# Kernel tuning notes

Measured on AMD Instinct MI355X. Metric: run time of the kernel, lower is better.

Reference implementation:

```python
import jax, jax.numpy as jnp
import numpy as np

B, N, NS, C, H = 2, 2048, 2048, 512, 8
HD = C // H
SCALE = HD ** -0.5
NEG = -10000.0


def setup_inputs() -> dict:
    key = jax.random.key(0)
    ks = jax.random.split(key, 9)
    q = jax.random.normal(ks[0], (B, N, C), dtype=jnp.float32)
    k = jax.random.normal(ks[1], (B, NS, C), dtype=jnp.float32)
    v = jax.random.normal(ks[2], (B, NS, C), dtype=jnp.float32)
    # 1.0 marks invalid support positions (gets -10000 added)
    supp_valid_mask = (jax.random.uniform(ks[3], (B, NS)) < 0.2).astype(jnp.float32)
    # binary fg/bg support mask used for cycle consistency
    supp_mask = jax.random.randint(ks[4], (B, NS), 0, 2, dtype=jnp.int32)
    w = 0.02
    Wq = jax.random.normal(ks[5], (C, C), dtype=jnp.float32) * w
    Wk = jax.random.normal(ks[6], (C, C), dtype=jnp.float32) * w
    Wv = jax.random.normal(ks[7], (C, C), dtype=jnp.float32) * w
    Wproj = jax.random.normal(ks[8], (C, C), dtype=jnp.float32) * w
    return {"q": q, "k": k, "v": v, "supp_valid_mask": supp_valid_mask,
            "supp_mask": supp_mask, "Wq": Wq, "Wk": Wk, "Wv": Wv, "Wproj": Wproj}


def reference(q, k, v, supp_valid_mask, supp_mask, Wq, Wk, Wv, Wproj):
    b, n, c = q.shape
    ns = k.shape[1]
    # linear projections (torch Linear: x @ W^T), split heads -> [B,H,N,HD]
    qh = (q @ Wq.T).reshape(b, n, H, HD).transpose(0, 2, 1, 3)
    kh = (k @ Wk.T).reshape(b, ns, H, HD).transpose(0, 2, 1, 3)
    vh = (v @ Wv.T).reshape(b, ns, H, HD).transpose(0, 2, 1, 3)
    attn = jnp.einsum('bhnd,bhmd->bhnm', qh, kh) * SCALE  # [B,H,N,NS]

    # cycle-consistency association (vectorized over heads)
    k2q = jnp.argmax(attn, axis=2)                    # [B,H,NS] idx into N
    q2k = jnp.argmax(attn, axis=3)                    # [B,H,N]  idx into NS
    re_map_idx = jnp.take_along_axis(q2k, k2q, axis=2)  # [B,H,NS]
    sm = jnp.broadcast_to(supp_mask[:, None, :], (b, H, ns))
    re_map_mask = jnp.take_along_axis(sm, re_map_idx, axis=2)
    asso = sm == re_map_mask                          # [B,H,NS] bool

    # mark cycle-inconsistent positions invalid (eval: ass_drop is identity)
    valid = jnp.broadcast_to(supp_valid_mask[:, None, :], (b, H, ns))
    valid = jnp.where(asso, valid, 1.0)

    attn = attn + (valid * NEG)[:, :, None, :]
    attn = jax.nn.softmax(attn, axis=-1)
    x = jnp.einsum('bhnm,bhmd->bhnd', attn, vh)       # [B,H,N,HD]
    x = x.transpose(0, 2, 1, 3).reshape(b, n, c)
    return x @ Wproj.T
```

## Files before the change

kernel.cpp:

```cpp
#include <hip/hip_runtime.h>
#include <hip/hip_bf16.h>
#include <stdint.h>

#define H_ 8
#define NS_ 2048
#define C_ 512
#define HD_ 64
#define SCALE_ 0.125f
#define NEG_ -10000.0f
#define LOG2E_ 1.4426950408889634f
#define MFIX_ 4.0f

typedef _Float16 f16x8_t __attribute__((ext_vector_type(8)));
typedef _Float16 f16x4_t __attribute__((ext_vector_type(4)));
typedef float f32x4_t __attribute__((ext_vector_type(4)));

#define MFMAH(a, b, c) __builtin_amdgcn_mfma_f32_16x16x32_f16(a, b, c, 0, 0, 0)

__device__ inline f16x8_t load_h8(const _Float16* p) {
    return *reinterpret_cast<const f16x8_t*>(p);
}

__device__ inline void gload_lds16(const void* g, void* l) {
    __builtin_amdgcn_global_load_lds(
        (const __attribute__((address_space(1))) unsigned int*)g,
        (__attribute__((address_space(3))) unsigned int*)l, 16, 0, 0);
}

__device__ inline unsigned orderF(float v) {
    unsigned u = __float_as_uint(v);
    return (u & 0x80000000u) ? ~u : (u | 0x80000000u);
}
__device__ inline unsigned long long packVR(float v, int idx) {
    return ((unsigned long long)orderF(v) << 32) | (unsigned)(~idx);
}
__device__ inline unsigned long long max64(unsigned long long a, unsigned long long b) {
    return a > b ? a : b;
}
__device__ inline unsigned long long shflx64(unsigned long long x, int m) {
    unsigned lo = (unsigned)x, hi = (unsigned)(x >> 32);
    lo = __shfl_xor(lo, m, 64);
    hi = __shfl_xor(hi, m, 64);
    return ((unsigned long long)hi << 32) | lo;
}

__global__ __launch_bounds__(256) void wsplit4(
        const float* __restrict__ w0, const float* __restrict__ w1,
        const float* __restrict__ w2, const float* __restrict__ w3,
        _Float16* __restrict__ hi, _Float16* __restrict__ lo)
{
    const int i = blockIdx.x * 256 + threadIdx.x;
    const int y = blockIdx.y;
    const float* src = (y == 0) ? w0 : (y == 1) ? w1 : (y == 2) ? w2 : w3;
    const float4 v = reinterpret_cast<const float4*>(src)[i];
    f16x4_t hv, lv;
    hv[0] = (_Float16)v.x; hv[1] = (_Float16)v.y;
    hv[2] = (_Float16)v.z; hv[3] = (_Float16)v.w;
    lv[0] = (_Float16)(v.x - (float)hv[0]);
    lv[1] = (_Float16)(v.y - (float)hv[1]);
    lv[2] = (_Float16)(v.z - (float)hv[2]);
    lv[3] = (_Float16)(v.w - (float)hv[3]);
    const size_t o = ((size_t)y << 16) + i;
    reinterpret_cast<f16x4_t*>(hi)[o] = hv;
    reinterpret_cast<f16x4_t*>(lo)[o] = lv;
}

__global__ __launch_bounds__(256) void proj_gemm(
        const float* __restrict__ qin, const float* __restrict__ kin,
        const float* __restrict__ vin,
        const _Float16* __restrict__ wHall, const _Float16* __restrict__ wLall,
        _Float16* __restrict__ qhi, _Float16* __restrict__ qlo,
        _Float16* __restrict__ khi, _Float16* __restrict__ klo,
        _Float16* __restrict__ vT)
{
    __shared__ __attribute__((aligned(16))) _Float16 Wsh[2][2][4096];
    const int zz = blockIdx.z;
    const float* A32 = (zz == 0) ? qin : (zz == 1) ? kin : vin;
    const _Float16* Wh = wHall + ((size_t)zz << 18);
    const _Float16* Wl = wLall + ((size_t)zz << 18);
    const int t = threadIdx.x, w = t >> 6, lane = t & 63;
    const int m16 = lane & 15, quad = lane >> 4;
    const int bm = blockIdx.x << 7, bn = blockIdx.y << 6;
    const int r0 = bm + (w << 5) + m16, r1 = r0 + 16;
    const int krow = lane >> 3, kblk = (lane & 7) ^ (krow & 7);
    const int e = m16 & 7;
    const int s00 = (quad ^ e) << 3, s01 = ((4 + quad) ^ e) << 3;
    const f32x4_t z = {0.f, 0.f, 0.f, 0.f};
    f32x4_t acc[2][4];
    #pragma unroll
    for (int rs = 0; rs < 2; rs++)
        #pragma unroll
        for (int tl = 0; tl < 4; tl++) acc[rs][tl] = z;

    auto stageW = [&](int buf, int kc) {
        #pragma unroll
        for (int ci = 0; ci < 4; ci++) {
            const int pp = (w << 2) + ci;
            const int s = pp >> 3, pj = pp & 7;
            const _Float16* src = (s ? Wl : Wh)
                + (size_t)(bn + (pj << 3) + krow) * C_ + kc + (kblk << 3);
            gload_lds16(src, &Wsh[buf][s][pj << 9]);
        }
    };
    auto loadA = [&](int kc, f16x8_t* d) {
        #pragma unroll
        for (int rs = 0; rs < 2; rs++) {
            const float* pr = A32 + (size_t)(rs ? r1 : r0) * C_ + kc + (quad << 3);
            #pragma unroll
            for (int seg = 0; seg < 2; seg++) {
                f16x8_t hv, lv;
                #pragma unroll
                for (int i = 0; i < 8; i++) {
                    const float x = pr[seg * 32 + i];
                    const _Float16 hh = (_Float16)x;
                    hv[i] = hh;
                    lv[i] = (_Float16)(x - (float)hh);
                }
                d[rs * 4 + seg] = hv;
                d[rs * 4 + seg + 2] = lv;
            }
        }
    };

    f16x8_t cA[8], nA[8];
    stageW(0, 0);
    loadA(0, cA);
    for (int ch = 0; ch < 8; ch++) {
        __syncthreads();
        if (ch + 1 < 8) {
            stageW((ch + 1) & 1, (ch + 1) << 6);
            loadA((ch + 1) << 6, nA);
        }
        const _Float16* W0 = Wsh[ch & 1][0];
        const _Float16* W1 = Wsh[ch & 1][1];
        #pragma unroll
        for (int tl = 0; tl < 4; tl++) {
            const int j64 = ((tl << 4) + m16) << 6;
            const f16x8_t bh0 = load_h8(&W0[j64 + s00]);
            const f16x8_t bh1 = load_h8(&W0[j64 + s01]);
            const f16x8_t bl0 = load_h8(&W1[j64 + s00]);
            const f16x8_t bl1 = load_h8(&W1[j64 + s01]);
            f32x4_t c0 = acc[0][tl];
            c0 = MFMAH(cA[0], bh0, c0); c0 = MFMAH(cA[1], bh1, c0);
            c0 = MFMAH(cA[2], bh0, c0); c0 = MFMAH(cA[3], bh1, c0);
            c0 = MFMAH(cA[0], bl0, c0); c0 = MFMAH(cA[1], bl1, c0);
            acc[0][tl] = c0;
            f32x4_t c1 = acc[1][tl];
            c1 = MFMAH(cA[4], bh0, c1); c1 = MFMAH(cA[5], bh1, c1);
            c1 = MFMAH(cA[6], bh0, c1); c1 = MFMAH(cA[7], bh1, c1);
            c1 = MFMAH(cA[4], bl0, c1); c1 = MFMAH(cA[5], bl1, c1);
            acc[1][tl] = c1;
        }
        #pragma unroll
        for (int i = 0; i < 8; i++) cA[i] = nA[i];
    }
    const int by = blockIdx.y;
    _Float16* o1 = (zz == 0) ? qhi : khi;
    _Float16* o2 = (zz == 0) ? qlo : klo;
    #pragma unroll
    for (int rs = 0; rs < 2; rs++) {
        #pragma unroll
        for (int tl = 0; tl < 4; tl++) {
            #pragma unroll
            for (int r = 0; r < 4; r++) {
                const int gr = bm + (w << 5) + (rs << 4) + (quad << 2) + r;
                const float val = acc[rs][tl][r];
                const int b = gr >> 11, n = gr & 2047;
                const int d = (tl << 4) + m16;
                const int bh = (b << 3) + by;
                if (zz == 2) {
                    vT[(((size_t)((bh << 6) + (n >> 5)) << 6) + d) * 32 + (n & 31)] = (_Float16)val;
                } else {
                    const size_t idx = ((((size_t)bh << 11) + n) << 6) + d;
                    const _Float16 hh = (_Float16)val;
                    o1[idx] = hh;
                    o2[idx] = (_Float16)(val - (float)hh);
                }
            }
        }
    }
}

__global__ __launch_bounds__(256) void argmax_mfma(
        const _Float16* __restrict__ qhi, const _Float16* __restrict__ qlo,
        const _Float16* __restrict__ khi, const _Float16* __restrict__ klo,
        unsigned long long* __restrict__ rowP, unsigned long long* __restrict__ colP)
{
    __shared__ __attribute__((aligned(16))) _Float16 Ksh[2][2][4096];
    __shared__ unsigned long long colbest[1024];
    const int bx = blockIdx.x;
    const int bh = ((bx & 7) << 1) | (bx >> 8);
    const int rt = (bx >> 3) & 15;
    const int ks = (bx >> 7) & 1;
    const int t = threadIdx.x, w = t >> 6, lane = t & 63;
    const int m16 = lane & 15, quad = lane >> 4;
    const int wrow = (rt << 7) + (w << 5);
    const size_t qoff0 = ((((size_t)bh << 11) + wrow + m16) << 6) + (quad << 3);
    const size_t qoff1 = qoff0 + 1024;
    const f16x8_t a00h = load_h8(qhi + qoff0), a01h = load_h8(qhi + qoff0 + 32);
    const f16x8_t a00l = load_h8(qlo + qoff0), a01l = load_h8(qlo + qoff0 + 32);
    const f16x8_t a10h = load_h8(qhi + qoff1), a11h = load_h8(qhi + qoff1 + 32);
    const f16x8_t a10l = load_h8(qlo + qoff1), a11l = load_h8(qlo + qoff1 + 32);
    for (int c = t; c < 1024; c += 256) colbest[c] = 0;
    const int krow = lane >> 3, kblk = (lane & 7) ^ (krow & 7);
    const int e = m16 & 7;
    const int s00 = (quad ^ e) << 3, s01 = ((4 + quad) ^ e) << 3;
    const size_t kbase = (((size_t)bh << 11) + (ks << 10)) << 6;
    float bv0[4] = {-3.4e38f, -3.4e38f, -3.4e38f, -3.4e38f};
    float bv1[4] = {-3.4e38f, -3.4e38f, -3.4e38f, -3.4e38f};
    int bc0[4] = {0, 0, 0, 0}, bc1[4] = {0, 0, 0, 0};
    const f32x4_t z = {0.f, 0.f, 0.f, 0.f};

    auto stage = [&](int buf, int cidx) {
        const size_t ce = kbase + ((size_t)cidx << 12);
        #pragma unroll
        for (int ci = 0; ci < 4; ci++) {
            const int pp = (w << 2) + ci;
            const int s = pp >> 3, pj = pp & 7;
            const _Float16* src = (s ? klo : khi) + ce + (((pj << 3) + krow) << 6) + (kblk << 3);
            gload_lds16(src, &Ksh[buf][s][pj << 9]);
        }
    };

    stage(0, 0);
    for (int ch = 0; ch < 16; ch++) {
        __syncthreads();
        if (ch + 1 < 16) stage((ch + 1) & 1, ch + 1);
        const _Float16* K0 = Ksh[ch & 1][0];
        const _Float16* K1 = Ksh[ch & 1][1];
        const int kc0 = (ks << 10) + (ch << 6);
        #pragma unroll
        for (int tl = 0; tl < 4; tl++) {
            const int j64 = ((tl << 4) + m16) << 6;
            const f16x8_t bh0 = load_h8(&K0[j64 + s00]);
            const f16x8_t bh1 = load_h8(&K0[j64 + s01]);
            const f16x8_t bl0 = load_h8(&K1[j64 + s00]);
            const f16x8_t bl1 = load_h8(&K1[j64 + s01]);
            f32x4_t c0 = MFMAH(a00h, bh0, z);
            c0 = MFMAH(a01h, bh1, c0);
            c0 = MFMAH(a00l, bh0, c0); c0 = MFMAH(a01l, bh1, c0);
            c0 = MFMAH(a00h, bl0, c0); c0 = MFMAH(a01h, bl1, c0);
            f32x4_t c1 = MFMAH(a10h, bh0, z);
            c1 = MFMAH(a11h, bh1, c1);
            c1 = MFMAH(a10l, bh0, c1); c1 = MFMAH(a11l, bh1, c1);
            c1 = MFMAH(a10h, bl0, c1); c1 = MFMAH(a11h, bl1, c1);
            const int gc = kc0 + (tl << 4) + m16;
            #pragma unroll
            for (int r = 0; r < 4; r++) {
                if (c0[r] > bv0[r]) { bv0[r] = c0[r]; bc0[r] = gc; }
                if (c1[r] > bv1[r]) { bv1[r] = c1[r]; bc1[r] = gc; }
            }
            float v = c0[0]; int ri = (quad << 2);
            if (c0[1] > v) { v = c0[1]; ri = (quad << 2) + 1; }
            if (c0[2] > v) { v = c0[2]; ri = (quad << 2) + 2; }
            if (c0[3] > v) { v = c0[3]; ri = (quad << 2) + 3; }
            if (c1[0] > v) { v = c1[0]; ri = 16 + (quad << 2); }
            if (c1[1] > v) { v = c1[1]; ri = 16 + (quad << 2) + 1; }
            if (c1[2] > v) { v = c1[2]; ri = 16 + (quad << 2) + 2; }
            if (c1[3] > v) { v = c1[3]; ri = 16 + (quad << 2) + 3; }
            unsigned long long pk = packVR(v, wrow + ri);
            pk = max64(pk, shflx64(pk, 16));
            pk = max64(pk, shflx64(pk, 32));
            if (quad == 0) atomicMax(&colbest[(ch << 6) + (tl << 4) + m16], pk);
        }
    }
    #pragma unroll
    for (int r = 0; r < 4; r++) {
        unsigned long long p0 = packVR(bv0[r], bc0[r]);
        p0 = max64(p0, shflx64(p0, 1)); p0 = max64(p0, shflx64(p0, 2));
        p0 = max64(p0, shflx64(p0, 4)); p0 = max64(p0, shflx64(p0, 8));
        if (m16 == 0)
            atomicMax(rowP + ((size_t)bh << 11) + wrow + (quad << 2) + r, p0);
        unsigned long long p1 = packVR(bv1[r], bc1[r]);
        p1 = max64(p1, shflx64(p1, 1)); p1 = max64(p1, shflx64(p1, 2));
        p1 = max64(p1, shflx64(p1, 4)); p1 = max64(p1, shflx64(p1, 8));
        if (m16 == 0)
            atomicMax(rowP + ((size_t)bh << 11) + wrow + 16 + (quad << 2) + r, p1);
    }
    __syncthreads();
    for (int c = t; c < 1024; c += 256)
        atomicMax(colP + ((size_t)bh << 11) + (ks << 10) + c, colbest[c]);
}

__global__ __launch_bounds__(256) void resolve(const unsigned long long* __restrict__ q2kP,
        const unsigned long long* __restrict__ k2qP, const int* __restrict__ supp_mask,
        const float* __restrict__ supp_valid, float* __restrict__ vn)
{
    const int t = blockIdx.x * 256 + threadIdx.x;
    const int bh = t >> 11, j = t & 2047, b = bh >> 3;
    const unsigned k2q = 0xFFFFFFFFu - (unsigned)(k2qP[t] & 0xFFFFFFFFull);
    const unsigned rm  = 0xFFFFFFFFu - (unsigned)(q2kP[(bh << 11) + k2q] & 0xFFFFFFFFull);
    const int asso = supp_mask[(b << 11) + j] == supp_mask[(b << 11) + (int)rm];
    const float valid = asso ? supp_valid[(b << 11) + j] : 1.0f;
    vn[t] = fmaf(valid, NEG_ * LOG2E_, -MFIX_);
}

__global__ __launch_bounds__(256) void attn_pv(
        const _Float16* __restrict__ qh, const _Float16* __restrict__ kh,
        const _Float16* __restrict__ vT, const float* __restrict__ vnG,
        float* __restrict__ xp, float* __restrict__ lp)
{
    __shared__ __attribute__((aligned(16))) _Float16 Ksh[2][2048];
    __shared__ __attribute__((aligned(16))) _Float16 Vsh[2][2048];
    __shared__ float vnL[1024];
    __shared__ __attribute__((aligned(16))) _Float16 pbuf[4][2][640];
    const int bx = blockIdx.x;
    const int bh = ((bx & 7) << 1) | (bx >> 8);
    const int rt = (bx >> 3) & 15;
    const int ks = (bx >> 7) & 1;
    const int t = threadIdx.x, w = t >> 6, lane = t & 63;
    const int m16 = lane & 15, quad = lane >> 4;
    const int rowbase = (rt << 7) + (w << 5);
    const size_t qoff0 = ((((size_t)bh << 11) + rowbase + m16) << 6) + (quad << 3);
    const size_t qoff1 = qoff0 + 1024;
    const f16x8_t a0 = load_h8(qh + qoff0), a1 = load_h8(qh + qoff0 + 32);
    const f16x8_t a2 = load_h8(qh + qoff1), a3 = load_h8(qh + qoff1 + 32);
    for (int c = t; c < 1024; c += 256) vnL[c] = vnG[(bh << 11) + (ks << 10) + c];
    const float KS = SCALE_ * LOG2E_;
    const int krow = lane >> 3, kblk = (lane & 7) ^ ((lane >> 3) & 7);
    const int vrow = lane >> 2, vblk = (lane & 3) ^ ((lane >> 3) & 3);
    const int e = m16 & 7;
    const int s00 = (quad ^ e) << 3, s01 = ((4 + quad) ^ e) << 3;
    const int vsw = (m16 >> 1) & 3;
    const f32x4_t z = {0.f, 0.f, 0.f, 0.f};
    f32x4_t xa0[4], xa1[4];
    #pragma unroll
    for (int nt = 0; nt < 4; nt++) { xa0[nt] = z; xa1[nt] = z; }
    float lr0[4] = {0.f, 0.f, 0.f, 0.f}, lr1[4] = {0.f, 0.f, 0.f, 0.f};
    const size_t kbel = ((size_t)bh << 11) * HD_;
    _Float16* pw0 = pbuf[w][0];
    _Float16* pw1 = pbuf[w][1];

    auto stage = [&](int buf, int ch) {
        const int kcg = (ks << 10) + (ch << 5);
        const size_t ce = kbel + (size_t)kcg * HD_;
        const size_t ve = ((size_t)(bh << 6) + (kcg >> 5)) << 11;
        #pragma unroll
        for (int ci = 0; ci < 2; ci++) {
            const int call = (w << 1) + ci;
            if (call < 4) {
                const _Float16* src = kh + ce + ((call * 8 + krow) << 6) + (kblk << 3);
                gload_lds16(src, &Ksh[buf][call << 9]);
            } else {
                const int j = call - 4;
                const _Float16* src = vT + ve + ((j * 16 + vrow) << 5) + (vblk << 3);
                gload_lds16(src, &Vsh[buf][j << 9]);
            }
        }
    };

    stage(0, 0);
    for (int ch = 0; ch < 32; ch++) {
        __syncthreads();
        if (ch + 1 < 32) stage((ch + 1) & 1, ch + 1);
        const _Float16* K = Ksh[ch & 1];
        const _Float16* V = Vsh[ch & 1];
        const f16x8_t b00 = load_h8(&K[(m16 << 6) + s00]);
        const f16x8_t b01 = load_h8(&K[(m16 << 6) + s01]);
        const f16x8_t b10 = load_h8(&K[((16 + m16) << 6) + s00]);
        const f16x8_t b11 = load_h8(&K[((16 + m16) << 6) + s01]);
        f32x4_t c00 = MFMAH(a0, b00, z); c00 = MFMAH(a1, b01, c00);
        f32x4_t c01 = MFMAH(a0, b10, z); c01 = MFMAH(a1, b11, c01);
        f32x4_t c10 = MFMAH(a2, b00, z); c10 = MFMAH(a3, b01, c10);
        f32x4_t c11 = MFMAH(a2, b10, z); c11 = MFMAH(a3, b11, c11);
        const float vn0 = vnL[(ch << 5) + m16], vn1 = vnL[(ch << 5) + 16 + m16];
        #pragma unroll
        for (int r = 0; r < 4; r++) {
            const float p00 = exp2f(fmaf(c00[r], KS, vn0));
            const float p01 = exp2f(fmaf(c01[r], KS, vn1));
            lr0[r] += p00 + p01;
            pw0[(((quad << 2) + r) * 40) + m16]      = (_Float16)p00;
            pw0[(((quad << 2) + r) * 40) + 16 + m16] = (_Float16)p01;
            const float p10 = exp2f(fmaf(c10[r], KS, vn0));
            const float p11 = exp2f(fmaf(c11[r], KS, vn1));
            lr1[r] += p10 + p11;
            pw1[(((quad << 2) + r) * 40) + m16]      = (_Float16)p10;
            pw1[(((quad << 2) + r) * 40) + 16 + m16] = (_Float16)p11;
        }
        __threadfence_block();
        const f16x8_t pa0 = load_h8(&pw0[m16 * 40 + (quad << 3)]);
        const f16x8_t pa1 = load_h8(&pw1[m16 * 40 + (quad << 3)]);
        #pragma unroll
        for (int nt = 0; nt < 4; nt++) {
            const f16x8_t vb = load_h8(&V[((nt * 16 + m16) << 5) + ((quad ^ vsw) << 3)]);
            xa0[nt] = MFMAH(pa0, vb, xa0[nt]);
            xa1[nt] = MFMAH(pa1, vb, xa1[nt]);
        }
    }
    #pragma unroll
    for (int d = 1; d < 16; d <<= 1) {
        #pragma unroll
        for (int r = 0; r < 4; r++) {
            lr0[r] += __shfl_xor(lr0[r], d, 64);
            lr1[r] += __shfl_xor(lr1[r], d, 64);
        }
    }
    const int b = bh >> 3, h = bh & 7;
    if (m16 == 0) {
        #pragma unroll
        for (int r = 0; r < 4; r++) {
            lp[((size_t)ks << 15) + (bh << 11) + rowbase + (quad << 2) + r] = lr0[r];
            lp[((size_t)ks << 15) + (bh << 11) + rowbase + 16 + (quad << 2) + r] = lr1[r];
        }
    }
    const size_t xbase = ((size_t)ks << 21);
    #pragma unroll
    for (int r = 0; r < 4; r++) {
        const int row0 = rowbase + (quad << 2) + r;
        const int row1 = row0 + 16;
        #pragma unroll
        for (int nt = 0; nt < 4; nt++) {
            xp[xbase + (((size_t)(b << 11) + row0) << 9) + (h << 6) + (nt << 4) + m16] = xa0[nt][r];
            xp[xbase + (((size_t)(b << 11) + row1) << 9) + (h << 6) + (nt << 4) + m16] = xa1[nt][r];
        }
    }
}

__global__ __launch_bounds__(256) void out_gemm(
        const float* __restrict__ xp, const float* __restrict__ lp,
        const _Float16* __restrict__ Wh, const _Float16* __restrict__ Wl,
        float* __restrict__ outF)
{
    __shared__ __attribute__((aligned(16))) _Float16 Wsh[2][2][4096];
    const int t = threadIdx.x, w = t >> 6, lane = t & 63;
    const int m16 = lane & 15, quad = lane >> 4;
    const int bm = blockIdx.x << 7, bn = blockIdx.y << 6;
    const int r0 = bm + (w << 5) + m16, r1 = r0 + 16;
    const int krow = lane >> 3, kblk = (lane & 7) ^ (krow & 7);
    const int e = m16 & 7;
    const int s00 = (quad ^ e) << 3, s01 = ((4 + quad) ^ e) << 3;
    const f32x4_t z = {0.f, 0.f, 0.f, 0.f};
    f32x4_t acc[2][4];
    #pragma unroll
    for (int rs = 0; rs < 2; rs++)
        #pragma unroll
        for (int tl = 0; tl < 4; tl++) acc[rs][tl] = z;

    auto stageW = [&](int buf, int kc) {
        #pragma unroll
        for (int ci = 0; ci < 4; ci++) {
            const int pp = (w << 2) + ci;
            const int s = pp >> 3, pj = pp & 7;
            const _Float16* src = (s ? Wl : Wh)
                + (size_t)(bn + (pj << 3) + krow) * C_ + kc + (kblk << 3);
            gload_lds16(src, &Wsh[buf][s][pj << 9]);
        }
    };
    auto loadA = [&](int ch, f16x8_t* d) {
        const int kc = ch << 6;
        #pragma unroll
        for (int rs = 0; rs < 2; rs++) {
            const int r = rs ? r1 : r0;
            const int b = r >> 11, n = r & 2047;
            const size_t li = ((size_t)((b << 3) + ch) << 11) + n;
            const float linv = 1.0f / (lp[li] + lp[32768 + li]);
            const size_t base = ((size_t)r << 9) + kc + (quad << 3);
            #pragma unroll
            for (int seg = 0; seg < 2; seg++) {
                f16x8_t hv, lv;
                #pragma unroll
                for (int i = 0; i < 8; i++) {
                    const size_t o = base + seg * 32 + i;
                    const float x = (xp[o] + xp[2097152 + o]) * linv;
                    const _Float16 hh = (_Float16)x;
                    hv[i] = hh;
                    lv[i] = (_Float16)(x - (float)hh);
                }
                d[rs * 4 + seg] = hv;
                d[rs * 4 + seg + 2] = lv;
            }
        }
    };

    f16x8_t cA[8], nA[8];
    stageW(0, 0);
    loadA(0, cA);
    for (int ch = 0; ch < 8; ch++) {
        __syncthreads();
        if (ch + 1 < 8) {
            stageW((ch + 1) & 1, (ch + 1) << 6);
            loadA(ch + 1, nA);
        }
        const _Float16* W0 = Wsh[ch & 1][0];
        const _Float16* W1 = Wsh[ch & 1][1];
        #pragma unroll
        for (int tl = 0; tl < 4; tl++) {
            const int j64 = ((tl << 4) + m16) << 6;
            const f16x8_t bh0 = load_h8(&W0[j64 + s00]);
            const f16x8_t bh1 = load_h8(&W0[j64 + s01]);
            const f16x8_t bl0 = load_h8(&W1[j64 + s00]);
            const f16x8_t bl1 = load_h8(&W1[j64 + s01]);
            f32x4_t c0 = acc[0][tl];
            c0 = MFMAH(cA[0], bh0, c0); c0 = MFMAH(cA[1], bh1, c0);
            c0 = MFMAH(cA[2], bh0, c0); c0 = MFMAH(cA[3], bh1, c0);
            c0 = MFMAH(cA[0], bl0, c0); c0 = MFMAH(cA[1], bl1, c0);
            acc[0][tl] = c0;
            f32x4_t c1 = acc[1][tl];
            c1 = MFMAH(cA[4], bh0, c1); c1 = MFMAH(cA[5], bh1, c1);
            c1 = MFMAH(cA[6], bh0, c1); c1 = MFMAH(cA[7], bh1, c1);
            c1 = MFMAH(cA[4], bl0, c1); c1 = MFMAH(cA[5], bl1, c1);
            acc[1][tl] = c1;
        }
        #pragma unroll
        for (int i = 0; i < 8; i++) cA[i] = nA[i];
    }
    #pragma unroll
    for (int rs = 0; rs < 2; rs++) {
        #pragma unroll
        for (int tl = 0; tl < 4; tl++) {
            #pragma unroll
            for (int r = 0; r < 4; r++) {
                const int gr = bm + (w << 5) + (rs << 4) + (quad << 2) + r;
                const int gj = bn + (tl << 4) + m16;
                outF[(size_t)gr * C_ + gj] = acc[rs][tl][r];
            }
        }
    }
}

extern "C" void kernel_launch(void* const* d_in, const int* in_sizes, int n_in,
                              void* d_out, int out_size, void* d_ws, size_t ws_size,
                              hipStream_t stream) {
    const float* q  = (const float*)d_in[0];
    const float* k  = (const float*)d_in[1];
    const float* v  = (const float*)d_in[2];
    const float* supp_valid = (const float*)d_in[3];
    const int*   supp_mask  = (const int*)d_in[4];
    const float* Wq = (const float*)d_in[5];
    const float* Wk = (const float*)d_in[6];
    const float* Wv = (const float*)d_in[7];
    const float* Wp = (const float*)d_in[8];
    float* out = (float*)d_out;

    char* p = (char*)d_ws;
    _Float16* qhi = (_Float16*)p;      p += 4194304;
    _Float16* qlo = (_Float16*)p;      p += 4194304;
    _Float16* khi = (_Float16*)p;      p += 4194304;
    _Float16* klo = (_Float16*)p;      p += 4194304;
    _Float16* vT  = (_Float16*)p;      p += 4194304;
    float* xp     = (float*)p;         p += 16777216;
    _Float16* wH  = (_Float16*)p;      p += 2097152;
    _Float16* wL  = (_Float16*)p;      p += 2097152;
    unsigned long long* q2kP = (unsigned long long*)p; p += 262144;
    unsigned long long* k2qP = (unsigned long long*)p; p += 262144;
    float* lp = (float*)p;             p += 262144;
    float* validNeg = (float*)p;       p += 131072;

    hipMemsetAsync(q2kP, 0, 524288, stream);

    dim3 bG(256);
    wsplit4<<<dim3(256, 4), bG, 0, stream>>>(Wq, Wk, Wv, Wp, wH, wL);
    proj_gemm<<<dim3(32, 8, 3), bG, 0, stream>>>(q, k, v, wH, wL,
                                                 qhi, qlo, khi, klo, vT);

    argmax_mfma<<<512, bG, 0, stream>>>(qhi, qlo, khi, klo, q2kP, k2qP);

    resolve<<<128, bG, 0, stream>>>(q2kP, k2qP, supp_mask, supp_valid, validNeg);

    attn_pv<<<512, bG, 0, stream>>>(qhi, khi, vT, validNeg, xp, lp);

    out_gemm<<<dim3(32, 8), bG, 0, stream>>>(xp, lp,
                                             wH + 3 * 262144, wL + 3 * 262144, out);
}
```

Baseline: 234.1 us.

## Double grid for argmax and attention, compute row sums via MFMA

The argmax kernel now splits the key dimension into four chunks instead of two, and the attention kernel handles 16 rows per wave instead of 32. Both launch 1024 blocks instead of 512, which raises parallelism on a GPU with many CUs. In attention the softmax row sums come from an MFMA against a ones vector rather than shuffle reductions, and P is stored as packed half pairs, with V's key order permuted to match. The cost is more redundant K/V staging per row and more atomics on the column partials.

```diff
diff --git a/kernel.cpp b/kernel.cpp
--- a/kernel.cpp
+++ b/kernel.cpp
@@ -169,7 +169,8 @@
                 const int d = (tl << 4) + m16;
                 const int bh = (b << 3) + by;
                 if (zz == 2) {
-                    vT[(((size_t)((bh << 6) + (n >> 5)) << 6) + d) * 32 + (n & 31)] = (_Float16)val;
+                    const int kp = ((n & 15) << 1) | ((n >> 4) & 1);
+                    vT[(((size_t)((bh << 6) + (n >> 5)) << 6) + d) * 32 + kp] = (_Float16)val;
                 } else {
                     const size_t idx = ((((size_t)bh << 11) + n) << 6) + d;
                     const _Float16 hh = (_Float16)val;
@@ -187,11 +188,12 @@
         unsigned long long* __restrict__ rowP, unsigned long long* __restrict__ colP)
 {
     __shared__ __attribute__((aligned(16))) _Float16 Ksh[2][2][4096];
-    __shared__ unsigned long long colbest[1024];
+    __shared__ unsigned long long colbest[512];
     const int bx = blockIdx.x;
-    const int bh = ((bx & 7) << 1) | (bx >> 8);
-    const int rt = (bx >> 3) & 15;
-    const int ks = (bx >> 7) & 1;
+    const int bh = ((bx & 7) << 1) | (bx >> 9);
+    const int mid = (bx >> 3) & 63;
+    const int rt = mid & 15;
+    const int ks = mid >> 4;
     const int t = threadIdx.x, w = t >> 6, lane = t & 63;
     const int m16 = lane & 15, quad = lane >> 4;
     const int wrow = (rt << 7) + (w << 5);
@@ -201,11 +203,11 @@
     const f16x8_t a00l = load_h8(qlo + qoff0), a01l = load_h8(qlo + qoff0 + 32);
     const f16x8_t a10h = load_h8(qhi + qoff1), a11h = load_h8(qhi + qoff1 + 32);
     const f16x8_t a10l = load_h8(qlo + qoff1), a11l = load_h8(qlo + qoff1 + 32);
-    for (int c = t; c < 1024; c += 256) colbest[c] = 0;
+    for (int c = t; c < 512; c += 256) colbest[c] = 0;
     const int krow = lane >> 3, kblk = (lane & 7) ^ (krow & 7);
     const int e = m16 & 7;
     const int s00 = (quad ^ e) << 3, s01 = ((4 + quad) ^ e) << 3;
-    const size_t kbase = (((size_t)bh << 11) + (ks << 10)) << 6;
+    const size_t kbase = (((size_t)bh << 11) + (ks << 9)) << 6;
     float bv0[4] = {-3.4e38f, -3.4e38f, -3.4e38f, -3.4e38f};
     float bv1[4] = {-3.4e38f, -3.4e38f, -3.4e38f, -3.4e38f};
     int bc0[4] = {0, 0, 0, 0}, bc1[4] = {0, 0, 0, 0};
@@ -223,12 +225,12 @@
     };
 
     stage(0, 0);
-    for (int ch = 0; ch < 16; ch++) {
+    for (int ch = 0; ch < 8; ch++) {
         __syncthreads();
-        if (ch + 1 < 16) stage((ch + 1) & 1, ch + 1);
+        if (ch + 1 < 8) stage((ch + 1) & 1, ch + 1);
         const _Float16* K0 = Ksh[ch & 1][0];
         const _Float16* K1 = Ksh[ch & 1][1];
-        const int kc0 = (ks << 10) + (ch << 6);
+        const int kc0 = (ks << 9) + (ch << 6);
         #pragma unroll
         for (int tl = 0; tl < 4; tl++) {
             const int j64 = ((tl << 4) + m16) << 6;
@@ -278,8 +280,8 @@
             atomicMax(rowP + ((size_t)bh << 11) + wrow + 16 + (quad << 2) + r, p1);
     }
     __syncthreads();
-    for (int c = t; c < 1024; c += 256)
-        atomicMax(colP + ((size_t)bh << 11) + (ks << 10) + c, colbest[c]);
+    for (int c = t; c < 512; c += 256)
+        atomicMax(colP + ((size_t)bh << 11) + (ks << 9) + c, colbest[c]);
 }
 
 __global__ __launch_bounds__(256) void resolve(const unsigned long long* __restrict__ q2kP,
@@ -303,18 +305,16 @@
     __shared__ __attribute__((aligned(16))) _Float16 Ksh[2][2048];
     __shared__ __attribute__((aligned(16))) _Float16 Vsh[2][2048];
     __shared__ float vnL[1024];
-    __shared__ __attribute__((aligned(16))) _Float16 pbuf[4][2][640];
+    __shared__ __attribute__((aligned(16))) unsigned pbuf[4][320];
     const int bx = blockIdx.x;
-    const int bh = ((bx & 7) << 1) | (bx >> 8);
-    const int rt = (bx >> 3) & 15;
-    const int ks = (bx >> 7) & 1;
+    const int bh = ((bx & 7) << 1) | (bx >> 9);
+    const int mid = (bx >> 3) & 63;
+    const int rt = mid & 31, ks = mid >> 5;
     const int t = threadIdx.x, w = t >> 6, lane = t & 63;
     const int m16 = lane & 15, quad = lane >> 4;
-    const int rowbase = (rt << 7) + (w << 5);
-    const size_t qoff0 = ((((size_t)bh << 11) + rowbase + m16) << 6) + (quad << 3);
-    const size_t qoff1 = qoff0 + 1024;
-    const f16x8_t a0 = load_h8(qh + qoff0), a1 = load_h8(qh + qoff0 + 32);
-    const f16x8_t a2 = load_h8(qh + qoff1), a3 = load_h8(qh + qoff1 + 32);
+    const int rowbase = (rt << 6) + (w << 4);
+    const size_t qoff = ((((size_t)bh << 11) + rowbase + m16) << 6) + (quad << 3);
+    const f16x8_t a0 = load_h8(qh + qoff), a1 = load_h8(qh + qoff + 32);
     for (int c = t; c < 1024; c += 256) vnL[c] = vnG[(bh << 11) + (ks << 10) + c];
     const float KS = SCALE_ * LOG2E_;
     const int krow = lane >> 3, kblk = (lane & 7) ^ ((lane >> 3) & 7);
@@ -322,14 +322,16 @@
     const int e = m16 & 7;
     const int s00 = (quad ^ e) << 3, s01 = ((4 + quad) ^ e) << 3;
     const int vsw = (m16 >> 1) & 3;
+    f16x8_t ones;
+    #pragma unroll
+    for (int i = 0; i < 8; i++) ones[i] = (_Float16)1.0f;
     const f32x4_t z = {0.f, 0.f, 0.f, 0.f};
-    f32x4_t xa0[4], xa1[4];
-    #pragma unroll
-    for (int nt = 0; nt < 4; nt++) { xa0[nt] = z; xa1[nt] = z; }
-    float lr0[4] = {0.f, 0.f, 0.f, 0.f}, lr1[4] = {0.f, 0.f, 0.f, 0.f};
+    f32x4_t xacc[4];
+    #pragma unroll
+    for (int nt = 0; nt < 4; nt++) xacc[nt] = z;
+    f32x4_t lacc = z;
     const size_t kbel = ((size_t)bh << 11) * HD_;
-    _Float16* pw0 = pbuf[w][0];
-    _Float16* pw1 = pbuf[w][1];
+    unsigned* pw = pbuf[w];
 
     auto stage = [&](int buf, int ch) {
         const int kcg = (ks << 10) + (ch << 5);
@@ -359,60 +361,40 @@
         const f16x8_t b01 = load_h8(&K[(m16 << 6) + s01]);
         const f16x8_t b10 = load_h8(&K[((16 + m16) << 6) + s00]);
         const f16x8_t b11 = load_h8(&K[((16 + m16) << 6) + s01]);
-        f32x4_t c00 = MFMAH(a0, b00, z); c00 = MFMAH(a1, b01, c00);
-        f32x4_t c01 = MFMAH(a0, b10, z); c01 = MFMAH(a1, b11, c01);
-        f32x4_t c10 = MFMAH(a2, b00, z); c10 = MFMAH(a3, b01, c10);
-        f32x4_t c11 = MFMAH(a2, b10, z); c11 = MFMAH(a3, b11, c11);
+        f32x4_t c0 = MFMAH(a0, b00, z); c0 = MFMAH(a1, b01, c0);
+        f32x4_t c1 = MFMAH(a0, b10, z); c1 = MFMAH(a1, b11, c1);
         const float vn0 = vnL[(ch << 5) + m16], vn1 = vnL[(ch << 5) + 16 + m16];
         #pragma unroll
         for (int r = 0; r < 4; r++) {
-            const float p00 = exp2f(fmaf(c00[r], KS, vn0));
-            const float p01 = exp2f(fmaf(c01[r], KS, vn1));
-            lr0[r] += p00 + p01;
-            pw0[(((quad << 2) + r) * 40) + m16]      = (_Float16)p00;
-            pw0[(((quad << 2) + r) * 40) + 16 + m16] = (_Float16)p01;
-            const float p10 = exp2f(fmaf(c10[r], KS, vn0));
-            const float p11 = exp2f(fmaf(c11[r], KS, vn1));
-            lr1[r] += p10 + p11;
-            pw1[(((quad << 2) + r) * 40) + m16]      = (_Float16)p10;
-            pw1[(((quad << 2) + r) * 40) + 16 + m16] = (_Float16)p11;
+            const float p0 = exp2f(fmaf(c0[r], KS, vn0));
+            const float p1 = exp2f(fmaf(c1[r], KS, vn1));
+            union { _Float16 h[2]; unsigned u; } pk_;
+            pk_.h[0] = (_Float16)p0;
+            pk_.h[1] = (_Float16)p1;
+            pw[((quad << 2) + r) * 20 + m16] = pk_.u;
         }
         __threadfence_block();
-        const f16x8_t pa0 = load_h8(&pw0[m16 * 40 + (quad << 3)]);
-        const f16x8_t pa1 = load_h8(&pw1[m16 * 40 + (quad << 3)]);
+        const f16x8_t pa = *reinterpret_cast<const f16x8_t*>(&pw[m16 * 20 + (quad << 2)]);
+        lacc = MFMAH(pa, ones, lacc);
         #pragma unroll
         for (int nt = 0; nt < 4; nt++) {
             const f16x8_t vb = load_h8(&V[((nt * 16 + m16) << 5) + ((quad ^ vsw) << 3)]);
-            xa0[nt] = MFMAH(pa0, vb, xa0[nt]);
-            xa1[nt] = MFMAH(pa1, vb, xa1[nt]);
-        }
-    }
-    #pragma unroll
-    for (int d = 1; d < 16; d <<= 1) {
-        #pragma unroll
-        for (int r = 0; r < 4; r++) {
-            lr0[r] += __shfl_xor(lr0[r], d, 64);
-            lr1[r] += __shfl_xor(lr1[r], d, 64);
+            xacc[nt] = MFMAH(pa, vb, xacc[nt]);
         }
     }
     const int b = bh >> 3, h = bh & 7;
     if (m16 == 0) {
         #pragma unroll
-        for (int r = 0; r < 4; r++) {
-            lp[((size_t)ks << 15) + (bh << 11) + rowbase + (quad << 2) + r] = lr0[r];
-            lp[((size_t)ks << 15) + (bh << 11) + rowbase + 16 + (quad << 2) + r] = lr1[r];
-        }
+        for (int r = 0; r < 4; r++)
+            lp[((size_t)ks << 15) + (bh << 11) + rowbase + (quad << 2) + r] = lacc[r];
     }
     const size_t xbase = ((size_t)ks << 21);
     #pragma unroll
     for (int r = 0; r < 4; r++) {
-        const int row0 = rowbase + (quad << 2) + r;
-        const int row1 = row0 + 16;
-        #pragma unroll
-        for (int nt = 0; nt < 4; nt++) {
-            xp[xbase + (((size_t)(b << 11) + row0) << 9) + (h << 6) + (nt << 4) + m16] = xa0[nt][r];
-            xp[xbase + (((size_t)(b << 11) + row1) << 9) + (h << 6) + (nt << 4) + m16] = xa1[nt][r];
-        }
+        const int row = rowbase + (quad << 2) + r;
+        #pragma unroll
+        for (int nt = 0; nt < 4; nt++)
+            xp[xbase + (((size_t)(b << 11) + row) << 9) + (h << 6) + (nt << 4) + m16] = xacc[nt][r];
     }
 }
 
@@ -553,11 +535,11 @@
     proj_gemm<<<dim3(32, 8, 3), bG, 0, stream>>>(q, k, v, wH, wL,
                                                  qhi, qlo, khi, klo, vT);
 
-    argmax_mfma<<<512, bG, 0, stream>>>(qhi, qlo, khi, klo, q2kP, k2qP);
+    argmax_mfma<<<1024, bG, 0, stream>>>(qhi, qlo, khi, klo, q2kP, k2qP);
 
     resolve<<<128, bG, 0, stream>>>(q2kP, k2qP, supp_mask, supp_valid, validNeg);
 
-    attn_pv<<<512, bG, 0, stream>>>(qhi, khi, vT, validNeg, xp, lp);
+    attn_pv<<<1024, bG, 0, stream>>>(qhi, khi, vT, validNeg, xp, lp);
 
     out_gemm<<<dim3(32, 8), bG, 0, stream>>>(xp, lp,
                                              wH + 3 * 262144, wL + 3 * 262144, out);
```

Result: faster. 221.9 us (-5.2%).
